# Performance work log

Measured on AMD Instinct MI355X. Metric: run time of the kernel, lower is better.

## Reference

```python
import jax, jax.numpy as jnp
import numpy as np

B, N, D_IN, D_OUT = 4096, 200, 64, 64


def setup_inputs() -> dict:
    key = jax.random.key(0)
    k1, k2 = jax.random.split(key)
    x = jax.random.normal(k1, (B, N, D_IN), dtype=jnp.float32)
    # weight initialized like TF add_weight default (glorot-ish scale via normal here)
    weight = jax.random.normal(k2, (1, N, D_IN, D_OUT), dtype=jnp.float32) * (1.0 / np.sqrt(D_IN))
    bias = jnp.zeros((1, N, D_OUT), dtype=jnp.float32)
    return {"x": x, "weight": weight, "bias": bias}


def reference(x, weight, bias):
    # Original: (x[..., None] * weight).sum(-2) + bias
    # == per-token matmul: out[b,n,o] = sum_i x[b,n,i] * weight[0,n,i,o] + bias[0,n,o]
    out = jnp.einsum('bni,nio->bno', x, weight[0])
    return out + bias
```

## Files before the change

### kernel.cpp

```cpp
#include <hip/hip_runtime.h>


#define B_DIM 4096
#define N_DIM 200
#define D 64

typedef __attribute__((ext_vector_type(8))) short bf16x8;
typedef __attribute__((ext_vector_type(4))) float f32x4;

__device__ __forceinline__ unsigned bf16_rne(float f) {
  unsigned u = __float_as_uint(f);
  return (u + 0x7fffu + ((u >> 16) & 1u)) >> 16;
}

__device__ __forceinline__ void cvt_split8(const float4 a, const float4 b,
                                           bf16x8& h, bf16x8& l) {
  float f[8] = {a.x, a.y, a.z, a.w, b.x, b.y, b.z, b.w};
#pragma unroll
  for (int j = 0; j < 8; ++j) {
    const unsigned hb = bf16_rne(f[j]);
    const float r = f[j] - __uint_as_float(hb << 16);
    const unsigned lb = bf16_rne(r);
    h[j] = (short)hb;
    l[j] = (short)lb;
  }
}

__global__ __launch_bounds__(256, 2)
void nlinear_mfma(const float* __restrict__ x,
                  const float* __restrict__ w,
                  const float* __restrict__ bias,
                  float* __restrict__ out) {
  const int n    = blockIdx.y;
  const int tid  = threadIdx.x;
  const int lane = tid & 63;
  const int wave = tid >> 6;
  const int c    = lane & 15;
  const int kg   = lane >> 4;

  __shared__ float w_lds[D * D];
  __shared__ float b_lds[D];

  {
    const float4* src = (const float4*)(w + (size_t)n * (D * D));
    float4* dst = (float4*)w_lds;
#pragma unroll
    for (int k = 0; k < 4; ++k) dst[tid + 256 * k] = src[tid + 256 * k];
    if (tid < 16)
      ((float4*)b_lds)[tid] = ((const float4*)(bias + (size_t)n * D))[tid];
  }
  __syncthreads();

  bf16x8 Wh[2][4], Wl[2][4];
#pragma unroll
  for (int ks = 0; ks < 2; ++ks) {
#pragma unroll
    for (int nf = 0; nf < 4; ++nf) {
#pragma unroll
      for (int j = 0; j < 8; ++j) {
        const int i = ks * 32 + kg * 8 + j;
        const float v = w_lds[i * D + nf * 16 + c];
        const unsigned hb = bf16_rne(v);
        const float r = v - __uint_as_float(hb << 16);
        const unsigned lb = bf16_rne(r);
        Wh[ks][nf][j] = (short)hb;
        Wl[ks][nf][j] = (short)lb;
      }
    }
  }

  const size_t rstride = (size_t)N_DIM * D;
  const int row0 = blockIdx.x * 256 + wave * 64;
  const float* xb = x + (size_t)row0 * rstride + (size_t)n * D;
  float* ob = out + (size_t)row0 * rstride + (size_t)n * D;

  const float bv[4] = {b_lds[c], b_lds[16 + c], b_lds[32 + c], b_lds[48 + c]};

#pragma unroll
  for (int mf = 0; mf < 4; ++mf) {
    const float* xr = xb + (size_t)(mf * 16 + c) * rstride + kg * 8;
    const float4 v0 = *(const float4*)(xr);
    const float4 v1 = *(const float4*)(xr + 4);
    const float4 v2 = *(const float4*)(xr + 32);
    const float4 v3 = *(const float4*)(xr + 36);
    bf16x8 ah[2], al[2];
    cvt_split8(v0, v1, ah[0], al[0]);
    cvt_split8(v2, v3, ah[1], al[1]);

    f32x4 acc[4];
#pragma unroll
    for (int nf = 0; nf < 4; ++nf) {
      f32x4 t = {bv[nf], bv[nf], bv[nf], bv[nf]};
      acc[nf] = t;
    }

#pragma unroll
    for (int ks = 0; ks < 2; ++ks) {
#pragma unroll
      for (int nf = 0; nf < 4; ++nf) {
        acc[nf] = __builtin_amdgcn_mfma_f32_16x16x32_bf16(ah[ks], Wh[ks][nf], acc[nf], 0, 0, 0);
        acc[nf] = __builtin_amdgcn_mfma_f32_16x16x32_bf16(ah[ks], Wl[ks][nf], acc[nf], 0, 0, 0);
        acc[nf] = __builtin_amdgcn_mfma_f32_16x16x32_bf16(al[ks], Wh[ks][nf], acc[nf], 0, 0, 0);
      }
    }

    float* orow = ob + (size_t)(mf * 16 + kg * 4) * rstride;
#pragma unroll
    for (int nf = 0; nf < 4; ++nf) {
#pragma unroll
      for (int j = 0; j < 4; ++j) {
        orow[(size_t)j * rstride + nf * 16 + c] = acc[nf][j];
      }
    }
  }
}

extern "C" void kernel_launch(void* const* d_in, const int* in_sizes, int n_in,
                              void* d_out, int out_size, void* d_ws, size_t ws_size,
                              hipStream_t stream) {
  const float* x    = (const float*)d_in[0];
  const float* w    = (const float*)d_in[1];
  const float* bias = (const float*)d_in[2];
  float*       out  = (float*)d_out;

  dim3 grid(B_DIM / 256, N_DIM);
  nlinear_mfma<<<grid, dim3(256), 0, stream>>>(x, w, bias, out);
}
```

Baseline: 373.5 us.

## Switch split-precision MFMA to fp16, prepack weights in workspace, prefetch x rows

Replaces the bf16 hi/lo split with an fp16 hi/lo split, using hardware conversions instead of manual bit rounding. Adds a separate w_prep kernel that converts the weights once per call into MFMA fragment layout in the workspace, so the main kernel loads them directly with no LDS staging or barrier. The main kernel also prefetches the next x row fragment while the current one is computed, and raises the occupancy hint to 4 blocks per SM. The fp16 split has a narrower exponent range than bf16, which is fine for these normal-distributed inputs but could lose accuracy for large or tiny values. The extra kernel launch adds fixed overhead.

```diff
diff --git a/kernel.cpp b/kernel.cpp
--- a/kernel.cpp
+++ b/kernel.cpp
@@ -4,32 +4,59 @@
 #define B_DIM 4096
 #define N_DIM 200
 #define D 64
+#define ROWS_PER_BLOCK 256
 
-typedef __attribute__((ext_vector_type(8))) short bf16x8;
+typedef __attribute__((ext_vector_type(8))) _Float16 half8;
 typedef __attribute__((ext_vector_type(4))) float f32x4;
 
-__device__ __forceinline__ unsigned bf16_rne(float f) {
-  unsigned u = __float_as_uint(f);
-  return (u + 0x7fffu + ((u >> 16) & 1u)) >> 16;
-}
-
-__device__ __forceinline__ void cvt_split8(const float4 a, const float4 b,
-                                           bf16x8& h, bf16x8& l) {
-  float f[8] = {a.x, a.y, a.z, a.w, b.x, b.y, b.z, b.w};
+__device__ __forceinline__ void split8(const float4 a, const float4 b,
+                                       half8& h, half8& l) {
+  const float f[8] = {a.x, a.y, a.z, a.w, b.x, b.y, b.z, b.w};
 #pragma unroll
   for (int j = 0; j < 8; ++j) {
-    const unsigned hb = bf16_rne(f[j]);
-    const float r = f[j] - __uint_as_float(hb << 16);
-    const unsigned lb = bf16_rne(r);
-    h[j] = (short)hb;
-    l[j] = (short)lb;
+    const _Float16 hh = (_Float16)f[j];
+    h[j] = hh;
+    l[j] = (_Float16)(f[j] - (float)hh);
   }
 }
 
-__global__ __launch_bounds__(256, 2)
-void nlinear_mfma(const float* __restrict__ x,
+__global__ __launch_bounds__(256)
+void w_prep(const float* __restrict__ w,
+            half8* __restrict__ wh, half8* __restrict__ wl) {
+  const int n    = blockIdx.x;
+  const int tid  = threadIdx.x;
+  const int lane = tid & 63;
+  const int g    = tid >> 6;
+  const int c    = lane & 15;
+  const int kg   = lane >> 4;
+  const float* wn = w + (size_t)n * (D * D);
+#pragma unroll
+  for (int t = 0; t < 2; ++t) {
+    const int combo = g * 2 + t;
+    const int ks = combo >> 2;
+    const int nf = combo & 3;
+    half8 h, l;
+#pragma unroll
+    for (int j = 0; j < 8; ++j) {
+      const int k = ks * 32 + kg * 8 + j;
+      const float v = wn[k * D + nf * 16 + c];
+      const _Float16 hh = (_Float16)v;
+      h[j] = hh;
+      l[j] = (_Float16)(v - (float)hh);
+    }
+    const size_t idx = ((size_t)(n * 2 + ks) * 4 + nf) * 64 + lane;
+    wh[idx] = h;
+    wl[idx] = l;
+  }
+}
+
+template <bool PREPPED>
+__global__ __launch_bounds__(256, 4)
+void nlinear_main(const float* __restrict__ x,
                   const float* __restrict__ w,
                   const float* __restrict__ bias,
+                  const half8* __restrict__ wh,
+                  const half8* __restrict__ wl,
                   float* __restrict__ out) {
   const int n    = blockIdx.y;
   const int tid  = threadIdx.x;
@@ -38,54 +65,59 @@
   const int c    = lane & 15;
   const int kg   = lane >> 4;
 
-  __shared__ float w_lds[D * D];
-  __shared__ float b_lds[D];
-
-  {
-    const float4* src = (const float4*)(w + (size_t)n * (D * D));
-    float4* dst = (float4*)w_lds;
+  half8 Wh[2][4], Wl[2][4];
+  if (PREPPED) {
 #pragma unroll
-    for (int k = 0; k < 4; ++k) dst[tid + 256 * k] = src[tid + 256 * k];
-    if (tid < 16)
-      ((float4*)b_lds)[tid] = ((const float4*)(bias + (size_t)n * D))[tid];
-  }
-  __syncthreads();
-
-  bf16x8 Wh[2][4], Wl[2][4];
+    for (int ks = 0; ks < 2; ++ks)
 #pragma unroll
-  for (int ks = 0; ks < 2; ++ks) {
+      for (int nf = 0; nf < 4; ++nf) {
+        const size_t idx = ((size_t)(n * 2 + ks) * 4 + nf) * 64 + lane;
+        Wh[ks][nf] = wh[idx];
+        Wl[ks][nf] = wl[idx];
+      }
+  } else {
+    const float* wn = w + (size_t)n * (D * D);
 #pragma unroll
-    for (int nf = 0; nf < 4; ++nf) {
+    for (int ks = 0; ks < 2; ++ks)
 #pragma unroll
-      for (int j = 0; j < 8; ++j) {
-        const int i = ks * 32 + kg * 8 + j;
-        const float v = w_lds[i * D + nf * 16 + c];
-        const unsigned hb = bf16_rne(v);
-        const float r = v - __uint_as_float(hb << 16);
-        const unsigned lb = bf16_rne(r);
-        Wh[ks][nf][j] = (short)hb;
-        Wl[ks][nf][j] = (short)lb;
-      }
-    }
+      for (int nf = 0; nf < 4; ++nf)
+#pragma unroll
+        for (int j = 0; j < 8; ++j) {
+          const float v = wn[(ks * 32 + kg * 8 + j) * D + nf * 16 + c];
+          const _Float16 hh = (_Float16)v;
+          Wh[ks][nf][j] = hh;
+          Wl[ks][nf][j] = (_Float16)(v - (float)hh);
+        }
   }
 
+  const float bv[4] = {bias[n * D + c],      bias[n * D + 16 + c],
+                       bias[n * D + 32 + c], bias[n * D + 48 + c]};
+
   const size_t rstride = (size_t)N_DIM * D;
-  const int row0 = blockIdx.x * 256 + wave * 64;
+  const int row0 = blockIdx.x * ROWS_PER_BLOCK + wave * 64;
   const float* xb = x + (size_t)row0 * rstride + (size_t)n * D;
   float* ob = out + (size_t)row0 * rstride + (size_t)n * D;
 
-  const float bv[4] = {b_lds[c], b_lds[16 + c], b_lds[32 + c], b_lds[48 + c]};
+  const float* xr0 = xb + (size_t)c * rstride + kg * 8;
+  float4 A0 = *(const float4*)(xr0);
+  float4 A1 = *(const float4*)(xr0 + 4);
+  float4 A2 = *(const float4*)(xr0 + 32);
+  float4 A3 = *(const float4*)(xr0 + 36);
 
-#pragma unroll
+#pragma unroll 1
   for (int mf = 0; mf < 4; ++mf) {
-    const float* xr = xb + (size_t)(mf * 16 + c) * rstride + kg * 8;
-    const float4 v0 = *(const float4*)(xr);
-    const float4 v1 = *(const float4*)(xr + 4);
-    const float4 v2 = *(const float4*)(xr + 32);
-    const float4 v3 = *(const float4*)(xr + 36);
-    bf16x8 ah[2], al[2];
-    cvt_split8(v0, v1, ah[0], al[0]);
-    cvt_split8(v2, v3, ah[1], al[1]);
+    const float4 v0 = A0, v1 = A1, v2 = A2, v3 = A3;
+    if (mf < 3) {
+      const float* xn = xb + (size_t)((mf + 1) * 16 + c) * rstride + kg * 8;
+      A0 = *(const float4*)(xn);
+      A1 = *(const float4*)(xn + 4);
+      A2 = *(const float4*)(xn + 32);
+      A3 = *(const float4*)(xn + 36);
+    }
+
+    half8 ah[2], al[2];
+    split8(v0, v1, ah[0], al[0]);
+    split8(v2, v3, ah[1], al[1]);
 
     f32x4 acc[4];
 #pragma unroll
@@ -95,23 +127,20 @@
     }
 
 #pragma unroll
-    for (int ks = 0; ks < 2; ++ks) {
+    for (int ks = 0; ks < 2; ++ks)
 #pragma unroll
       for (int nf = 0; nf < 4; ++nf) {
-        acc[nf] = __builtin_amdgcn_mfma_f32_16x16x32_bf16(ah[ks], Wh[ks][nf], acc[nf], 0, 0, 0);
-        acc[nf] = __builtin_amdgcn_mfma_f32_16x16x32_bf16(ah[ks], Wl[ks][nf], acc[nf], 0, 0, 0);
-        acc[nf] = __builtin_amdgcn_mfma_f32_16x16x32_bf16(al[ks], Wh[ks][nf], acc[nf], 0, 0, 0);
+        acc[nf] = __builtin_amdgcn_mfma_f32_16x16x32_f16(ah[ks], Wh[ks][nf], acc[nf], 0, 0, 0);
+        acc[nf] = __builtin_amdgcn_mfma_f32_16x16x32_f16(ah[ks], Wl[ks][nf], acc[nf], 0, 0, 0);
+        acc[nf] = __builtin_amdgcn_mfma_f32_16x16x32_f16(al[ks], Wh[ks][nf], acc[nf], 0, 0, 0);
       }
-    }
 
     float* orow = ob + (size_t)(mf * 16 + kg * 4) * rstride;
 #pragma unroll
-    for (int nf = 0; nf < 4; ++nf) {
+    for (int nf = 0; nf < 4; ++nf)
 #pragma unroll
-      for (int j = 0; j < 4; ++j) {
+      for (int j = 0; j < 4; ++j)
         orow[(size_t)j * rstride + nf * 16 + c] = acc[nf][j];
-      }
-    }
   }
 }
 
@@ -123,6 +152,16 @@
   const float* bias = (const float*)d_in[2];
   float*       out  = (float*)d_out;
 
-  dim3 grid(B_DIM / 256, N_DIM);
-  nlinear_mfma<<<grid, dim3(256), 0, stream>>>(x, w, bias, out);
+  const size_t NFRAGS = (size_t)N_DIM * 2 * 4 * 64;
+  const size_t NEED   = NFRAGS * 16 * 2;
+
+  dim3 grid(B_DIM / ROWS_PER_BLOCK, N_DIM);
+  if (d_ws && ws_size >= NEED) {
+    half8* wh = (half8*)d_ws;
+    half8* wl = wh + NFRAGS;
+    w_prep<<<dim3(N_DIM), dim3(256), 0, stream>>>(w, wh, wl);
+    nlinear_main<true><<<grid, dim3(256), 0, stream>>>(x, w, bias, wh, wl, out);
+  } else {
+    nlinear_main<false><<<grid, dim3(256), 0, stream>>>(x, w, bias, nullptr, nullptr, out);
+  }
 }
```

New measurement: 395.5 us. 1.06x slower.
